# Performance work log

Hardware: AMD Instinct MI355X
Metric: run time of the kernel (lower is better)

## Reference

```python
import jax, jax.numpy as jnp
import numpy as np

N_CLASSES = 4
GAMMA = 2.0
B, C, D, H, W = 2, 4, 64, 192, 192
INF = 1e12


def setup_inputs() -> dict:
    key = jax.random.key(0)
    k1, k2 = jax.random.split(key)
    inp = jax.random.normal(k1, (B, C, D, H, W), dtype=jnp.float32)
    tgt = jax.random.randint(k2, (B, 1, D, H, W), 0, N_CLASSES, dtype=jnp.int32)
    return {"input": inp, "target": tgt}


def _boundary(m):
    # m: bool [..., H, W]. Boundary pixel = in mask but not 4-connected interior
    # (image border counts as background, matching cv2.findContours contours).
    pad = [(0, 0)] * (m.ndim - 2) + [(1, 1), (1, 1)]
    p = jnp.pad(m, pad)
    up = p[..., :-2, 1:-1]
    down = p[..., 2:, 1:-1]
    left = p[..., 1:-1, :-2]
    right = p[..., 1:-1, 2:]
    interior = m & up & down & left & right
    return m & ~interior


def _edt_slices(seeds):
    # seeds: bool [N, H, W]. Exact 2D Euclidean distance to nearest seed pixel,
    # via separable brute-force squared-distance passes (Felzenszwalb-style).
    h, w = seeds.shape[-2:]
    iw = jnp.arange(w, dtype=jnp.float32)
    cw = (iw[:, None] - iw[None, :]) ** 2          # [W, W]
    ih = jnp.arange(h, dtype=jnp.float32)
    ch = (ih[:, None] - ih[None, :]) ** 2          # [H, H]

    def one(seed):
        f = jnp.where(seed, 0.0, INF)              # [H, W]
        # pass along W: g[h, i] = min_j f[h, j] + (i - j)^2
        g = jnp.min(f[:, None, :] + cw[None, :, :], axis=-1)   # [H, W]
        # pass along H: d2[i, w] = min_h (i - h)^2 + g[h, w]
        d2 = jnp.min(ch[:, :, None] + g[None, :, :], axis=1)   # [H, W]
        return jnp.sqrt(jnp.minimum(d2, INF))
    return jax.lax.map(one, seeds)


def _weight_map(pred, tgt):
    # pred, tgt: int [B, D, H, W]. Per-slice boundary-distance weight map.
    b, d, h, w = tgt.shape
    wmap = jnp.zeros((b, d, h, w), jnp.float32)
    for c in range(1, N_CLASSES):  # class 0 is skipped by the original loop
        gc = tgt == c
        pc = pred == c
        present = jnp.any(gc, axis=(-2, -1))                   # [B, D]
        bnd = _boundary(gc)
        dist = _edt_slices(bnd.reshape(b * d, h, w)).reshape(b, d, h, w)
        err = gc != pc
        wmap = wmap + jnp.where(err & present[..., None, None], dist, 0.0)
    # slices with no GT labels but some predicted foreground get weight 10
    empty = ~jnp.any(tgt != 0, axis=(-2, -1))                  # [B, D]
    wmap = wmap + jnp.where(empty[..., None, None] & (pred != 0), 10.0, 0.0)
    # per-slice min-max normalization, then exp(w) - 1, then + 1
    mn = jnp.min(wmap, axis=(-2, -1), keepdims=True)
    mx = jnp.max(wmap, axis=(-2, -1), keepdims=True)
    wmap = (wmap - mn) / (mx - mn + 1e-6)
    return jnp.exp(wmap)  # (exp(w) - 1) + 1


def reference(input, target):
    t = target[:, 0]                                            # [B, D, H, W]
    logp = jax.nn.log_softmax(input, axis=1)                    # [B, C, D, H, W]
    logpt = jnp.take_along_axis(logp, t[:, None], axis=1)[:, 0]  # [B, D, H, W]
    pt = jax.lax.stop_gradient(jnp.exp(logpt))                  # .data in torch
    pred = jnp.argmax(input, axis=1)                            # [B, D, H, W]
    wmap = jax.lax.stop_gradient(_weight_map(pred, t))
    loss = -((1.0 - pt) ** GAMMA) * (logpt * wmap)
    return jnp.sum(loss)  # size_average=False
```

## Files before the change

kernel.cpp:

```cpp
#include <hip/hip_runtime.h>
#include <math.h>

#define Bv 2
#define Cc 4
#define Dd 64
#define Hh 192
#define Ww 192
#define HW (Hh*Ww)
#define NSLICE (Bv*Dd)
#define NVOX ((size_t)NSLICE*HW)
#define DHW (Dd*HW)

typedef unsigned long long u64;

#define MROWSTRIDE 4
#define MASKU64 ((size_t)NSLICE*3*Hh*MROWSTRIDE)

__global__ __launch_bounds__(256) void prep_kernel(const float* __restrict__ inp,
    const int* __restrict__ tgt, unsigned char* __restrict__ tp,
    float* __restrict__ focal, u64* __restrict__ masks,
    unsigned int* __restrict__ flags) {
  int part  = blockIdx.x & 7;
  int slice = blockIdx.x >> 3;
  int b = slice >> 6, d = slice & 63;
  int wave = threadIdx.x >> 6, lane = threadIdx.x & 63;
  const float* c0 = inp + ((size_t)(b*Cc)*Dd + d)*HW;
  const float* c1 = c0 + DHW;
  const float* c2 = c0 + 2*DHW;
  const float* c3 = c0 + 3*DHW;
  const int*   tb = tgt + (size_t)slice*HW;
  unsigned int lbits = 0;

  for (int it = 0; it < 6; ++it) {
    int row = part*24 + wave*6 + it;
    int idx = row*Ww + lane*4;
    float4 x0, x1, x2, x3;
    int4 tv4 = make_int4(0,0,0,0), up4 = make_int4(-1,-1,-1,-1), dn4 = make_int4(-1,-1,-1,-1);
    if (lane < 48) {
      x0 = *(const float4*)(c0 + idx);
      x1 = *(const float4*)(c1 + idx);
      x2 = *(const float4*)(c2 + idx);
      x3 = *(const float4*)(c3 + idx);
      tv4 = *(const int4*)(tb + idx);
      if (row > 0)    up4 = *(const int4*)(tb + idx - Ww);
      if (row < Hh-1) dn4 = *(const int4*)(tb + idx + Ww);
    }
    int lf = __shfl(tv4.w, (lane-1)&63);
    int rt = __shfl(tv4.x, (lane+1)&63);
    unsigned nib1 = 0, nib2 = 0, nib3 = 0;
    if (lane < 48) {
      int tvs[4] = {tv4.x, tv4.y, tv4.z, tv4.w};
      int ups[4] = {up4.x, up4.y, up4.z, up4.w};
      int dns[4] = {dn4.x, dn4.y, dn4.z, dn4.w};
      int lfs[4] = {lf, tv4.x, tv4.y, tv4.z};
      int rts[4] = {tv4.y, tv4.z, tv4.w, rt};
      float a0[4] = {x0.x, x0.y, x0.z, x0.w};
      float a1[4] = {x1.x, x1.y, x1.z, x1.w};
      float a2[4] = {x2.x, x2.y, x2.z, x2.w};
      float a3[4] = {x3.x, x3.y, x3.z, x3.w};
      float4 fout;
      float* fo = (float*)&fout;
      unsigned pk4 = 0;
      #pragma unroll
      for (int k = 0; k < 4; ++k) {
        float xa = a0[k], xb = a1[k], xc = a2[k], xd = a3[k];
        int p = 0; float bst = xa;
        if (xb > bst) { bst = xb; p = 1; }
        if (xc > bst) { bst = xc; p = 2; }
        if (xd > bst) { bst = xd; p = 3; }
        int tv = tvs[k];
        float m = fmaxf(fmaxf(xa, xb), fmaxf(xc, xd));
        float e = expf(xa-m) + expf(xb-m) + expf(xc-m) + expf(xd-m);
        float xt = (tv==0) ? xa : (tv==1) ? xb : (tv==2) ? xc : xd;
        float logpt = xt - m - logf(e);
        float pt = expf(logpt);
        float om = 1.0f - pt;
        fo[k] = -(om*om)*logpt;
        pk4 |= (unsigned)(tv | (p << 4)) << (8*k);
        if (tv != 0) {
          lbits |= 1u << (tv-1);
          int col = lane*4 + k;
          bool interior = (row > 0) && (row < Hh-1) && (col > 0) && (col < Ww-1)
              && (ups[k]==tv) && (dns[k]==tv) && (lfs[k]==tv) && (rts[k]==tv);
          if (!interior) {
            if      (tv == 1) nib1 |= 1u << k;
            else if (tv == 2) nib2 |= 1u << k;
            else              nib3 |= 1u << k;
          }
        }
      }
      *(float4*)(focal + (size_t)slice*HW + idx) = fout;
      *(unsigned*)(tp + (size_t)slice*HW + idx) = pk4;
    }
    u64 m1 = (u64)nib1 << ((lane & 15)*4);
    u64 m2 = (u64)nib2 << ((lane & 15)*4);
    u64 m3 = (u64)nib3 << ((lane & 15)*4);
    #pragma unroll
    for (int off = 1; off < 16; off <<= 1) {
      m1 |= __shfl_xor(m1, off);
      m2 |= __shfl_xor(m2, off);
      m3 |= __shfl_xor(m3, off);
    }
    if (lane < 48 && (lane & 15) == 0) {
      int word = lane >> 4;
      size_t base = ((size_t)slice*3*Hh + row)*MROWSTRIDE + word;
      masks[base]                    = m1;
      masks[base + Hh*MROWSTRIDE]    = m2;
      masks[base + 2*Hh*MROWSTRIDE]  = m3;
    }
  }
  __shared__ unsigned int sb;
  if (threadIdx.x == 0) sb = 0u;
  __syncthreads();
  if (lbits) atomicOr(&sb, lbits);
  __syncthreads();
  if (threadIdx.x == 0 && sb) atomicOr(&flags[slice], sb);
}

__device__ __forceinline__ int nearest_bit_dist(u64 m0, u64 m1, u64 m2, int j) {
  int dr = 1<<20, dl = 1<<20;
  u64 r0, r1, r2;
  if (j >= 128)      { r0 = 0;  r1 = 0;  r2 = m2 & (~0ull << (j-128)); }
  else if (j >= 64)  { r0 = 0;  r1 = m1 & (~0ull << (j-64)); r2 = m2; }
  else               { r0 = m0 & (~0ull << j); r1 = m1; r2 = m2; }
  if      (r0) dr = (__ffsll((unsigned long long)r0) - 1) - j;
  else if (r1) dr = (__ffsll((unsigned long long)r1) + 63) - j;
  else if (r2) dr = (__ffsll((unsigned long long)r2) + 127) - j;
  u64 l0, l1, l2;
  if (j < 64)        { l0 = (j==63) ? m0 : (m0 & ((1ull<<(j+1))-1)); l1 = 0; l2 = 0; }
  else if (j < 128)  { l0 = m0; l1 = (j==127) ? m1 : (m1 & ((1ull<<(j-63))-1)); l2 = 0; }
  else               { l0 = m0; l1 = m1; l2 = (j==191) ? m2 : (m2 & ((1ull<<(j-127))-1)); }
  if      (l2) dl = j - (191 - __clzll((long long)l2));
  else if (l1) dl = j - (127 - __clzll((long long)l1));
  else if (l0) dl = j - (63  - __clzll((long long)l0));
  return dl < dr ? dl : dr;
}

__device__ __forceinline__ void push_items(unsigned short* list,
    unsigned int* cnt, bool want, unsigned val) {
  u64 mask = __ballot(want);
  if (mask == 0) return;
  int lane = threadIdx.x & 63;
  int total = __popcll(mask);
  int leader = __ffsll((long long)mask) - 1;
  unsigned b = 0;
  if (lane == leader) b = atomicAdd(cnt, (unsigned)total);
  b = __shfl(b, leader);
  if (want) {
    int off = __popcll(mask & ((1ull << lane) - 1));
    list[b + off] = (unsigned short)val;
  }
}

__global__ __launch_bounds__(256) void edt_kernel(const unsigned char* __restrict__ tp,
    const u64* __restrict__ masks, const unsigned int* __restrict__ flags,
    float* __restrict__ wmap, unsigned int* __restrict__ mnb,
    unsigned int* __restrict__ mxb) {
  __shared__ __align__(16) float wacc[2048];
  __shared__ unsigned short list[4096];
  __shared__ unsigned int cnt;
  __shared__ float smn[4], smx[4];
  int part  = blockIdx.x % 18;
  int slice = blockIdx.x / 18;
  unsigned int fl = flags[slice];
  bool empty = ((fl & 7u) == 0u);
  if (threadIdx.x == 0) cnt = 0u;
  __syncthreads();

  for (int it = 0; it < 2; ++it) {
    int lbase = it*1024 + threadIdx.x*4;
    unsigned pk = *(const unsigned*)(tp + (size_t)slice*HW + part*2048 + lbase);
    #pragma unroll
    for (int k = 0; k < 4; ++k) {
      int byte = (pk >> (8*k)) & 0xff;
      int tv = byte & 15, pv = byte >> 4;
      wacc[lbase+k] = (empty && pv != 0) ? 10.0f : 0.0f;
      bool diff = (tv != pv);
      bool w1 = diff && (tv >= 1) && ((fl >> (tv-1)) & 1u);
      bool w2 = diff && (pv >= 1) && ((fl >> (pv-1)) & 1u);
      push_items(list, &cnt, w1, (unsigned)(lbase+k) | ((unsigned)tv << 12));
      push_items(list, &cnt, w2, (unsigned)(lbase+k) | ((unsigned)pv << 12));
    }
  }
  __syncthreads();

  unsigned n = cnt;
  const u64* msl = masks + (size_t)slice*3*Hh*MROWSTRIDE;
  for (unsigned kk = threadIdx.x; kk < n; kk += 256) {
    unsigned item = list[kk];
    int lidx = item & 2047;
    int c = item >> 12;
    int idx = part*2048 + lidx;
    int i = idx / Ww, j = idx - i*Ww;
    const u64* M = msl + (size_t)(c-1)*Hh*MROWSTRIDE;
    int best = 1 << 30;
    for (int dr = 0; dr < Hh; ++dr) {
      int dr2 = dr*dr;
      if (dr2 >= best) break;
      int up = i - dr;
      if (up >= 0) {
        const u64* R = M + up*MROWSTRIDE;
        int dc = nearest_bit_dist(R[0], R[1], R[2], j);
        if (dc < (1<<20)) { int cand = dr2 + dc*dc; if (cand < best) best = cand; }
      }
      int dn = i + dr;
      if (dr && dn < Hh) {
        const u64* R = M + dn*MROWSTRIDE;
        int dc = nearest_bit_dist(R[0], R[1], R[2], j);
        if (dc < (1<<20)) { int cand = dr2 + dc*dc; if (cand < best) best = cand; }
      }
    }
    float dist = (best == (1 << 30)) ? 1.0e6f : sqrtf((float)best);
    atomicAdd(&wacc[lidx], dist);
  }
  __syncthreads();

  float lmn = 1.0e30f, lmx = 0.0f;
  for (int it = 0; it < 2; ++it) {
    int lbase = it*1024 + threadIdx.x*4;
    float4 wv = *(const float4*)&wacc[lbase];
    lmn = fminf(lmn, fminf(fminf(wv.x, wv.y), fminf(wv.z, wv.w)));
    lmx = fmaxf(lmx, fmaxf(fmaxf(wv.x, wv.y), fmaxf(wv.z, wv.w)));
    *(float4*)(wmap + (size_t)slice*HW + part*2048 + lbase) = wv;
  }
  for (int off = 32; off; off >>= 1) {
    lmn = fminf(lmn, __shfl_xor(lmn, off));
    lmx = fmaxf(lmx, __shfl_xor(lmx, off));
  }
  int wid = threadIdx.x >> 6;
  if ((threadIdx.x & 63) == 0) { smn[wid] = lmn; smx[wid] = lmx; }
  __syncthreads();
  if (threadIdx.x == 0) {
    lmn = fminf(fminf(smn[0], smn[1]), fminf(smn[2], smn[3]));
    lmx = fmaxf(fmaxf(smx[0], smx[1]), fmaxf(smx[2], smx[3]));
    atomicMin(&mnb[slice], __float_as_uint(lmn));
    atomicMax(&mxb[slice], __float_as_uint(lmx));
  }
}

__global__ __launch_bounds__(256) void loss_kernel(const float* __restrict__ focal,
    const float* __restrict__ wmap, const unsigned int* __restrict__ mnb,
    const unsigned int* __restrict__ mxb, float* __restrict__ out) {
  int part  = blockIdx.x % 9;
  int slice = blockIdx.x / 9;
  float mn = __uint_as_float(mnb[slice]);
  float mx = __uint_as_float(mxb[slice]);
  float inv = 1.0f/(mx - mn + 1e-6f);
  float acc = 0.0f;
  for (int it = 0; it < 4; ++it) {
    int idx = part*4096 + it*1024 + threadIdx.x*4;
    float4 f = *(const float4*)(focal + (size_t)slice*HW + idx);
    float4 w = *(const float4*)(wmap + (size_t)slice*HW + idx);
    acc += f.x * expf((w.x-mn)*inv);
    acc += f.y * expf((w.y-mn)*inv);
    acc += f.z * expf((w.z-mn)*inv);
    acc += f.w * expf((w.w-mn)*inv);
  }
  for (int off = 32; off; off >>= 1) acc += __shfl_xor(acc, off);
  __shared__ float sa[4];
  int wid = threadIdx.x >> 6;
  if ((threadIdx.x & 63) == 0) sa[wid] = acc;
  __syncthreads();
  if (threadIdx.x == 0) atomicAdd(out, sa[0]+sa[1]+sa[2]+sa[3]);
}

extern "C" void kernel_launch(void* const* d_in, const int* in_sizes, int n_in,
                              void* d_out, int out_size, void* d_ws, size_t ws_size,
                              hipStream_t stream) {
  const float* inp = (const float*)d_in[0];
  const int*   tgt = (const int*)d_in[1];
  char* ws = (char*)d_ws;
  unsigned char* tp    = (unsigned char*)ws;
  float*         focal = (float*)(ws + NVOX);
  float*         wmap  = (float*)(ws + 5*NVOX);
  u64*           masks = (u64*)(ws + 9*NVOX);
  unsigned int*  flags = (unsigned int*)(ws + 9*NVOX + MASKU64*8);
  unsigned int*  mxb   = flags + NSLICE;
  unsigned int*  mnb   = mxb + NSLICE;

  hipMemsetAsync(flags, 0, NSLICE*2*sizeof(unsigned int), stream);
  hipMemsetAsync(mnb, 0xFF, NSLICE*sizeof(unsigned int), stream);
  hipMemsetAsync(d_out, 0, sizeof(float), stream);

  prep_kernel<<<NSLICE*8, 256, 0, stream>>>(inp, tgt, tp, focal, masks, flags);
  edt_kernel<<<NSLICE*18, 256, 0, stream>>>(tp, masks, flags, wmap, mnb, mxb);
  loss_kernel<<<NSLICE*9, 256, 0, stream>>>(focal, wmap, mnb, mxb, (float*)d_out);
}
```

Baseline: 230.4 us.

## Tile EDT into 4-row blocks with LDS mask halo and drop memsets/atomics

The EDT kernel now processes 4-row tiles (48 per slice) and stages a ±12-row halo of the boundary bitmasks in shared memory, so nearby-row searches read LDS instead of global memory. Each pixel gets one list item carrying both candidate classes, which removes the shared atomicAdd on the accumulator. Per-block flags, min/max and partial sums are written to arrays and reduced later, including a new final reduction kernel, so the memsets and global atomics go away. The cost is more blocks with redundant halo loads, lower per-block occupancy with only 192 active threads in some phases, and one extra kernel launch.

```diff
diff --git a/kernel.cpp b/kernel.cpp
--- a/kernel.cpp
+++ b/kernel.cpp
@@ -16,20 +16,30 @@
 #define MROWSTRIDE 4
 #define MASKU64 ((size_t)NSLICE*3*Hh*MROWSTRIDE)
 
+#define TROWS 4
+#define TPX (TROWS*Ww)
+#define MARGIN 12
+#define SROWS (TROWS + 2*MARGIN)
+#define SSTRIDE 5
+#define NTILE (Hh/TROWS)
+
 __global__ __launch_bounds__(256) void prep_kernel(const float* __restrict__ inp,
     const int* __restrict__ tgt, unsigned char* __restrict__ tp,
     float* __restrict__ focal, u64* __restrict__ masks,
-    unsigned int* __restrict__ flags) {
+    unsigned int* __restrict__ flags8) {
   int part  = blockIdx.x & 7;
   int slice = blockIdx.x >> 3;
   int b = slice >> 6, d = slice & 63;
   int wave = threadIdx.x >> 6, lane = threadIdx.x & 63;
   const float* c0 = inp + ((size_t)(b*Cc)*Dd + d)*HW;
-  const float* c1 = c0 + DHW;
-  const float* c2 = c0 + 2*DHW;
-  const float* c3 = c0 + 3*DHW;
+  const float* c1p = c0 + DHW;
+  const float* c2p = c0 + 2*DHW;
+  const float* c3p = c0 + 3*DHW;
   const int*   tb = tgt + (size_t)slice*HW;
   unsigned int lbits = 0;
+  __shared__ unsigned int sb;
+  if (threadIdx.x == 0) sb = 0u;
+  __syncthreads();
 
   for (int it = 0; it < 6; ++it) {
     int row = part*24 + wave*6 + it;
@@ -38,9 +48,9 @@
     int4 tv4 = make_int4(0,0,0,0), up4 = make_int4(-1,-1,-1,-1), dn4 = make_int4(-1,-1,-1,-1);
     if (lane < 48) {
       x0 = *(const float4*)(c0 + idx);
-      x1 = *(const float4*)(c1 + idx);
-      x2 = *(const float4*)(c2 + idx);
-      x3 = *(const float4*)(c3 + idx);
+      x1 = *(const float4*)(c1p + idx);
+      x2 = *(const float4*)(c2p + idx);
+      x3 = *(const float4*)(c3p + idx);
       tv4 = *(const int4*)(tb + idx);
       if (row > 0)    up4 = *(const int4*)(tb + idx - Ww);
       if (row < Hh-1) dn4 = *(const int4*)(tb + idx + Ww);
@@ -109,12 +119,9 @@
       masks[base + 2*Hh*MROWSTRIDE]  = m3;
     }
   }
-  __shared__ unsigned int sb;
-  if (threadIdx.x == 0) sb = 0u;
-  __syncthreads();
   if (lbits) atomicOr(&sb, lbits);
   __syncthreads();
-  if (threadIdx.x == 0 && sb) atomicOr(&flags[slice], sb);
+  if (threadIdx.x == 0) flags8[blockIdx.x] = sb;
 }
 
 __device__ __forceinline__ int nearest_bit_dist(u64 m0, u64 m1, u64 m2, int j) {
@@ -136,8 +143,40 @@
   return dl < dr ? dl : dr;
 }
 
-__device__ __forceinline__ void push_items(unsigned short* list,
-    unsigned int* cnt, bool want, unsigned val) {
+__device__ __forceinline__ float edt_dist(const u64* __restrict__ smc,
+    const u64* __restrict__ gmc, int li, int i, int j) {
+  int best = 1 << 30;
+  for (int dr = 0; dr <= MARGIN; ++dr) {
+    if (dr*dr >= best) break;
+    const u64* R = smc + (li-dr)*SSTRIDE;
+    int dc = nearest_bit_dist(R[0], R[1], R[2], j);
+    if (dc < (1<<20)) { int cand = dr*dr + dc*dc; if (cand < best) best = cand; }
+    if (dr) {
+      const u64* R2 = smc + (li+dr)*SSTRIDE;
+      int dc2 = nearest_bit_dist(R2[0], R2[1], R2[2], j);
+      if (dc2 < (1<<20)) { int cand = dr*dr + dc2*dc2; if (cand < best) best = cand; }
+    }
+  }
+  for (int dr = MARGIN+1; dr < Hh; ++dr) {
+    if (dr*dr >= best) break;
+    int up = i - dr;
+    if (up >= 0) {
+      const u64* R = gmc + up*MROWSTRIDE;
+      int dc = nearest_bit_dist(R[0], R[1], R[2], j);
+      if (dc < (1<<20)) { int cand = dr*dr + dc*dc; if (cand < best) best = cand; }
+    }
+    int dn = i + dr;
+    if (dn < Hh) {
+      const u64* R = gmc + dn*MROWSTRIDE;
+      int dc = nearest_bit_dist(R[0], R[1], R[2], j);
+      if (dc < (1<<20)) { int cand = dr*dr + dc*dc; if (cand < best) best = cand; }
+    }
+  }
+  return (best == (1 << 30)) ? 1.0e6f : sqrtf((float)best);
+}
+
+__device__ __forceinline__ void push16(unsigned short* list, unsigned* cnt,
+    bool want, unsigned val) {
   u64 mask = __ballot(want);
   if (mask == 0) return;
   int lane = threadIdx.x & 63;
@@ -153,98 +192,113 @@
 }
 
 __global__ __launch_bounds__(256) void edt_kernel(const unsigned char* __restrict__ tp,
-    const u64* __restrict__ masks, const unsigned int* __restrict__ flags,
-    float* __restrict__ wmap, unsigned int* __restrict__ mnb,
-    unsigned int* __restrict__ mxb) {
-  __shared__ __align__(16) float wacc[2048];
-  __shared__ unsigned short list[4096];
-  __shared__ unsigned int cnt;
+    const u64* __restrict__ masks, const unsigned int* __restrict__ flags8,
+    float* __restrict__ wmap, float* __restrict__ mmn, float* __restrict__ mxx) {
+  __shared__ u64 sm[3*SROWS*SSTRIDE];
+  __shared__ __align__(16) float wacc[TPX];
+  __shared__ unsigned short list[TPX];
+  __shared__ unsigned cnt, sfl;
   __shared__ float smn[4], smx[4];
-  int part  = blockIdx.x % 18;
-  int slice = blockIdx.x / 18;
-  unsigned int fl = flags[slice];
+  int tile  = blockIdx.x % NTILE;
+  int slice = blockIdx.x / NTILE;
+  int r0 = tile*TROWS;
+  int tid = threadIdx.x;
+
+  if (tid == 0) {
+    unsigned f = 0;
+    #pragma unroll
+    for (int p = 0; p < 8; ++p) f |= flags8[slice*8 + p];
+    sfl = f; cnt = 0u;
+  }
+  __syncthreads();
+  unsigned fl = sfl;
   bool empty = ((fl & 7u) == 0u);
-  if (threadIdx.x == 0) cnt = 0u;
-  __syncthreads();
-
-  for (int it = 0; it < 2; ++it) {
-    int lbase = it*1024 + threadIdx.x*4;
-    unsigned pk = *(const unsigned*)(tp + (size_t)slice*HW + part*2048 + lbase);
+
+  for (int t = tid; t < 3*SROWS*3; t += 256) {
+    int c = t / (SROWS*3);
+    int rem = t - c*(SROWS*3);
+    int sr = rem / 3, w = rem - sr*3;
+    int gr = r0 - MARGIN + sr;
+    sm[(c*SROWS + sr)*SSTRIDE + w] = (gr >= 0 && gr < Hh)
+        ? masks[(((size_t)slice*3 + c)*Hh + gr)*MROWSTRIDE + w] : 0ull;
+  }
+
+  if (tid < 192) {
+    unsigned pk = *(const unsigned*)(tp + (size_t)slice*HW + r0*Ww + tid*4);
     #pragma unroll
     for (int k = 0; k < 4; ++k) {
+      int px = tid*4 + k;
       int byte = (pk >> (8*k)) & 0xff;
       int tv = byte & 15, pv = byte >> 4;
-      wacc[lbase+k] = (empty && pv != 0) ? 10.0f : 0.0f;
+      wacc[px] = (empty && pv != 0) ? 10.0f : 0.0f;
       bool diff = (tv != pv);
-      bool w1 = diff && (tv >= 1) && ((fl >> (tv-1)) & 1u);
-      bool w2 = diff && (pv >= 1) && ((fl >> (pv-1)) & 1u);
-      push_items(list, &cnt, w1, (unsigned)(lbase+k) | ((unsigned)tv << 12));
-      push_items(list, &cnt, w2, (unsigned)(lbase+k) | ((unsigned)pv << 12));
+      int cA, cB;
+      if (tv && pv) { cA = tv; cB = pv; } else { cA = tv | pv; cB = 0; }
+      int rl = px / Ww, j = px - rl*Ww;
+      push16(list, &cnt, diff,
+             (unsigned)j | ((unsigned)rl << 8) | ((unsigned)cA << 10) | ((unsigned)cB << 12));
     }
   }
   __syncthreads();
 
   unsigned n = cnt;
-  const u64* msl = masks + (size_t)slice*3*Hh*MROWSTRIDE;
-  for (unsigned kk = threadIdx.x; kk < n; kk += 256) {
+  const u64* gm0 = masks + (size_t)slice*3*Hh*MROWSTRIDE;
+  for (unsigned kk = tid; kk < n; kk += 256) {
     unsigned item = list[kk];
-    int lidx = item & 2047;
-    int c = item >> 12;
-    int idx = part*2048 + lidx;
-    int i = idx / Ww, j = idx - i*Ww;
-    const u64* M = msl + (size_t)(c-1)*Hh*MROWSTRIDE;
-    int best = 1 << 30;
-    for (int dr = 0; dr < Hh; ++dr) {
-      int dr2 = dr*dr;
-      if (dr2 >= best) break;
-      int up = i - dr;
-      if (up >= 0) {
-        const u64* R = M + up*MROWSTRIDE;
-        int dc = nearest_bit_dist(R[0], R[1], R[2], j);
-        if (dc < (1<<20)) { int cand = dr2 + dc*dc; if (cand < best) best = cand; }
-      }
-      int dn = i + dr;
-      if (dr && dn < Hh) {
-        const u64* R = M + dn*MROWSTRIDE;
-        int dc = nearest_bit_dist(R[0], R[1], R[2], j);
-        if (dc < (1<<20)) { int cand = dr2 + dc*dc; if (cand < best) best = cand; }
-      }
-    }
-    float dist = (best == (1 << 30)) ? 1.0e6f : sqrtf((float)best);
-    atomicAdd(&wacc[lidx], dist);
+    int j  = item & 255;
+    int rl = (item >> 8) & 3;
+    int cA = (item >> 10) & 3;
+    int cB = (item >> 12) & 3;
+    int i  = r0 + rl;
+    int li = MARGIN + rl;
+    float sum = 0.0f;
+    if (cA && ((fl >> (cA-1)) & 1u))
+      sum += edt_dist(sm + (cA-1)*SROWS*SSTRIDE, gm0 + (size_t)(cA-1)*Hh*MROWSTRIDE, li, i, j);
+    if (cB && ((fl >> (cB-1)) & 1u))
+      sum += edt_dist(sm + (cB-1)*SROWS*SSTRIDE, gm0 + (size_t)(cB-1)*Hh*MROWSTRIDE, li, i, j);
+    wacc[rl*Ww + j] += sum;
   }
   __syncthreads();
 
   float lmn = 1.0e30f, lmx = 0.0f;
-  for (int it = 0; it < 2; ++it) {
-    int lbase = it*1024 + threadIdx.x*4;
-    float4 wv = *(const float4*)&wacc[lbase];
-    lmn = fminf(lmn, fminf(fminf(wv.x, wv.y), fminf(wv.z, wv.w)));
-    lmx = fmaxf(lmx, fmaxf(fmaxf(wv.x, wv.y), fmaxf(wv.z, wv.w)));
-    *(float4*)(wmap + (size_t)slice*HW + part*2048 + lbase) = wv;
+  if (tid < 192) {
+    float4 wv = *(const float4*)&wacc[tid*4];
+    lmn = fminf(fminf(wv.x, wv.y), fminf(wv.z, wv.w));
+    lmx = fmaxf(fmaxf(wv.x, wv.y), fmaxf(wv.z, wv.w));
+    *(float4*)(wmap + (size_t)slice*HW + r0*Ww + tid*4) = wv;
   }
   for (int off = 32; off; off >>= 1) {
     lmn = fminf(lmn, __shfl_xor(lmn, off));
     lmx = fmaxf(lmx, __shfl_xor(lmx, off));
   }
-  int wid = threadIdx.x >> 6;
-  if ((threadIdx.x & 63) == 0) { smn[wid] = lmn; smx[wid] = lmx; }
-  __syncthreads();
-  if (threadIdx.x == 0) {
+  int wid = tid >> 6;
+  if ((tid & 63) == 0) { smn[wid] = lmn; smx[wid] = lmx; }
+  __syncthreads();
+  if (tid == 0) {
     lmn = fminf(fminf(smn[0], smn[1]), fminf(smn[2], smn[3]));
     lmx = fmaxf(fmaxf(smx[0], smx[1]), fmaxf(smx[2], smx[3]));
-    atomicMin(&mnb[slice], __float_as_uint(lmn));
-    atomicMax(&mxb[slice], __float_as_uint(lmx));
+    mmn[blockIdx.x] = lmn;
+    mxx[blockIdx.x] = lmx;
   }
 }
 
 __global__ __launch_bounds__(256) void loss_kernel(const float* __restrict__ focal,
-    const float* __restrict__ wmap, const unsigned int* __restrict__ mnb,
-    const unsigned int* __restrict__ mxb, float* __restrict__ out) {
+    const float* __restrict__ wmap, const float* __restrict__ mmn,
+    const float* __restrict__ mxx, float* __restrict__ pp) {
   int part  = blockIdx.x % 9;
   int slice = blockIdx.x / 9;
-  float mn = __uint_as_float(mnb[slice]);
-  float mx = __uint_as_float(mxb[slice]);
+  __shared__ float smm[2];
+  if (threadIdx.x < 64) {
+    float a = (threadIdx.x < NTILE) ? mmn[slice*NTILE + threadIdx.x] : 1.0e30f;
+    float c = (threadIdx.x < NTILE) ? mxx[slice*NTILE + threadIdx.x] : 0.0f;
+    for (int off = 32; off; off >>= 1) {
+      a = fminf(a, __shfl_xor(a, off));
+      c = fmaxf(c, __shfl_xor(c, off));
+    }
+    if (threadIdx.x == 0) { smm[0] = a; smm[1] = c; }
+  }
+  __syncthreads();
+  float mn = smm[0], mx = smm[1];
   float inv = 1.0f/(mx - mn + 1e-6f);
   float acc = 0.0f;
   for (int it = 0; it < 4; ++it) {
@@ -261,7 +315,19 @@
   int wid = threadIdx.x >> 6;
   if ((threadIdx.x & 63) == 0) sa[wid] = acc;
   __syncthreads();
-  if (threadIdx.x == 0) atomicAdd(out, sa[0]+sa[1]+sa[2]+sa[3]);
+  if (threadIdx.x == 0) pp[blockIdx.x] = sa[0]+sa[1]+sa[2]+sa[3];
+}
+
+__global__ __launch_bounds__(256) void final_kernel(const float* __restrict__ pp,
+    float* __restrict__ out) {
+  float acc = 0.0f;
+  for (int i = threadIdx.x; i < NSLICE*9; i += 256) acc += pp[i];
+  for (int off = 32; off; off >>= 1) acc += __shfl_xor(acc, off);
+  __shared__ float sa[4];
+  int wid = threadIdx.x >> 6;
+  if ((threadIdx.x & 63) == 0) sa[wid] = acc;
+  __syncthreads();
+  if (threadIdx.x == 0) out[0] = sa[0]+sa[1]+sa[2]+sa[3];
 }
 
 extern "C" void kernel_launch(void* const* d_in, const int* in_sizes, int n_in,
@@ -274,15 +340,13 @@
   float*         focal = (float*)(ws + NVOX);
   float*         wmap  = (float*)(ws + 5*NVOX);
   u64*           masks = (u64*)(ws + 9*NVOX);
-  unsigned int*  flags = (unsigned int*)(ws + 9*NVOX + MASKU64*8);
-  unsigned int*  mxb   = flags + NSLICE;
-  unsigned int*  mnb   = mxb + NSLICE;
-
-  hipMemsetAsync(flags, 0, NSLICE*2*sizeof(unsigned int), stream);
-  hipMemsetAsync(mnb, 0xFF, NSLICE*sizeof(unsigned int), stream);
-  hipMemsetAsync(d_out, 0, sizeof(float), stream);
-
-  prep_kernel<<<NSLICE*8, 256, 0, stream>>>(inp, tgt, tp, focal, masks, flags);
-  edt_kernel<<<NSLICE*18, 256, 0, stream>>>(tp, masks, flags, wmap, mnb, mxb);
-  loss_kernel<<<NSLICE*9, 256, 0, stream>>>(focal, wmap, mnb, mxb, (float*)d_out);
-}
+  unsigned int*  flags8 = (unsigned int*)(ws + 9*NVOX + MASKU64*8);
+  float*         mmn   = (float*)(flags8 + NSLICE*8);
+  float*         mxx   = mmn + NSLICE*48;
+  float*         pp    = mxx + NSLICE*48;
+
+  prep_kernel<<<NSLICE*8, 256, 0, stream>>>(inp, tgt, tp, focal, masks, flags8);
+  edt_kernel<<<NSLICE*NTILE, 256, 0, stream>>>(tp, masks, flags8, wmap, mmn, mxx);
+  loss_kernel<<<NSLICE*9, 256, 0, stream>>>(focal, wmap, mmn, mxx, pp);
+  final_kernel<<<1, 256, 0, stream>>>(pp, (float*)d_out);
+}
```

Measured after the change: 219.7 us. 4.6% less time.
